# Kernel optimization log

Hardware: AMD Instinct MI355X
Metric: run time of the kernel (lower is better)

The kernel has to match this reference:

```python
import jax, jax.numpy as jnp
import numpy as np

N_NODES = 50000
N_EDGES = 1600000
DIM = 128          # input_dim == hidden_dim == embed_dim
N_LAYERS = 5
NEG_SLOPE = 0.2    # PyG GATv2Conv default


def setup_inputs() -> dict:
    key = jax.random.key(0)
    ks = jax.random.split(key, 8)
    s = 1.0 / np.sqrt(DIM)
    x = jax.random.normal(ks[0], (N_NODES, DIM), dtype=jnp.float32)
    edge_index = jax.random.randint(ks[1], (2, N_EDGES), 0, N_NODES, dtype=jnp.int64)
    # stacked per-layer params (all dims are 128 so layers stack cleanly)
    Wl = jax.random.normal(ks[2], (N_LAYERS, DIM, DIM), dtype=jnp.float32) * s
    bl = jax.random.normal(ks[3], (N_LAYERS, DIM), dtype=jnp.float32) * 0.01
    Wr = jax.random.normal(ks[4], (N_LAYERS, DIM, DIM), dtype=jnp.float32) * s
    br = jax.random.normal(ks[5], (N_LAYERS, DIM), dtype=jnp.float32) * 0.01
    att = jax.random.normal(ks[6], (N_LAYERS, DIM), dtype=jnp.float32) * s
    bias = jax.random.normal(ks[7], (N_LAYERS, DIM), dtype=jnp.float32) * 0.01
    return {"x": x, "edge_index": edge_index, "Wl": Wl, "bl": bl,
            "Wr": Wr, "br": br, "att": att, "bias": bias}


def _gatv2_layer(x, src, dst, Wl, bl, Wr, br, att, bias):
    # x: [N, D]; src/dst: [E'] (self loops already appended)
    n = x.shape[0]
    xl = x @ Wl + bl                      # [N, D]  (source transform; also the message)
    xr = x @ Wr + br                      # [N, D]  (target transform)
    # per-edge GATv2 score: att . LeakyReLU(xl[src] + xr[dst])
    e = jax.nn.leaky_relu(xl[src] + xr[dst], NEG_SLOPE) @ att   # [E']
    # numerically stable segment-softmax over incoming edges of each dst node
    m = jax.ops.segment_max(e, dst, num_segments=n)
    m = jnp.where(jnp.isfinite(m), m, jnp.zeros_like(m))
    p = jnp.exp(e - m[dst])
    z = jax.ops.segment_sum(p, dst, num_segments=n)
    alpha = p / jnp.maximum(z[dst], jnp.asarray(1e-16, p.dtype))  # [E']
    out = jax.ops.segment_sum(alpha[:, None] * xl[src], dst, num_segments=n)
    return out + bias


def reference(x, edge_index, Wl, bl, Wr, br, att, bias):
    n = x.shape[0]
    # PyG GATv2Conv default add_self_loops=True; edges identical across layers -> append once
    loop = jnp.arange(n, dtype=edge_index.dtype)
    src = jnp.concatenate([edge_index[0], loop])
    dst = jnp.concatenate([edge_index[1], loop])
    h = x
    for i in range(N_LAYERS):
        h = _gatv2_layer(h, src, dst, Wl[i], bl[i], Wr[i], br[i], att[i], bias[i])
        if i < N_LAYERS - 1:
            h = jax.nn.relu(h)
    # global_mean_pool with batch=None -> mean over all nodes, shape [1, embed_dim]
    return jnp.mean(h, axis=0, keepdims=True)
```

## Files before the change

### kernel.cpp

```cpp
#include <hip/hip_runtime.h>
#include <hip/hip_bf16.h>

#define N_NODES 50000
#define N_EDGES 1600000
#define DIM 128
#define N_LAYERS 5
#define NEG 0.2f

#define NBKT 196
#define BCAP_A 9472
#define PBLK 98
#define EPB 16384
#define SEGCAP 12288
#define SENT N_NODES
#define LOG2E 1.4426950408889634f

typedef unsigned short u16;
typedef unsigned char u8;
typedef unsigned int u32;
using short8 = __attribute__((ext_vector_type(8))) short;
using f32x4  = __attribute__((ext_vector_type(4))) float;
typedef float f32x2 __attribute__((ext_vector_type(2)));

union FragU { uint4 u; short8 s; };

__device__ __forceinline__ f32x2 bf2v(u32 u) {
    union { u32 i; float f; } lo, hi;
    lo.i = u << 16;
    hi.i = u & 0xffff0000u;
    f32x2 r; r.x = lo.f; r.y = hi.f;
    return r;
}
__device__ __forceinline__ u16 f2bf(float f) {
    union { float f; u32 u; } v; v.f = f;
    u32 r = v.u + 0x7fffu + ((v.u >> 16) & 1u);
    return (u16)(r >> 16);
}
__device__ __forceinline__ u32 pk2(float a, float b) {
    return (u32)f2bf(a) | ((u32)f2bf(b) << 16);
}
__device__ __forceinline__ int clampi(int v) {
    v = (v < 0) ? 0 : v;
    return (v >= N_NODES) ? (N_NODES - 1) : v;
}
template<int CTRL>
__device__ __forceinline__ float rradd(float v) {
    int t = __builtin_amdgcn_update_dpp(0, __float_as_int(v), CTRL, 0xF, 0xF, true);
    return v + __int_as_float(t);
}

__global__ void k_probe(const int* __restrict__ ei32, int* __restrict__ flags,
                        int* __restrict__ bcnt) {
    __shared__ int cnt;
    int t = threadIdx.x;
    if (t == 0) cnt = 0;
    __syncthreads();
    if (ei32[2 * t + 1] == 0) atomicAdd(&cnt, 1);
    if (t < NBKT) bcnt[t] = 0;
    __syncthreads();
    if (t == 0) flags[0] = (cnt >= 255) ? 1 : 0;
}

__device__ __forceinline__ int ldidx(const void* ei, long long i, int m64) {
    int v = m64 ? (int)(((const long long*)ei)[i]) : ((const int*)ei)[i];
    return clampi(v);
}

__global__ void k_cvt_x(const float* __restrict__ x, u16* __restrict__ xb) {
    int i = blockIdx.x * 256 + threadIdx.x;
    float2 v = *(const float2*)(x + (size_t)i * 2);
    ((u32*)xb)[i] = pk2(v.x, v.y);
}

__global__ void k_cvt_w(const float* __restrict__ Wl, const float* __restrict__ Wr,
                        uint4* __restrict__ Wtg) {
    int id = blockIdx.x * 256 + threadIdx.x;
    if (id >= N_LAYERS * 16 * 256) return;
    int l = id >> 12;
    int rem = id & 4095;
    int kc = rem >> 8;
    int n = rem & 255;
    const float* W = (n < 128) ? (Wl + (size_t)l * DIM * DIM + n)
                               : (Wr + (size_t)l * DIM * DIM + (n - 128));
    u16 c[8];
#pragma unroll
    for (int j = 0; j < 8; ++j) c[j] = f2bf(W[(size_t)(kc * 8 + j) * DIM]);
    uint4 o;
    o.x = (u32)c[0] | ((u32)c[1] << 16);
    o.y = (u32)c[2] | ((u32)c[3] << 16);
    o.z = (u32)c[4] | ((u32)c[5] << 16);
    o.w = (u32)c[6] | ((u32)c[7] << 16);
    Wtg[(size_t)l * 4096 + n * 16 + (kc ^ (n & 15))] = o;
}

__global__ __launch_bounds__(1024) void k_part(
    const void* __restrict__ ei, const int* __restrict__ flags,
    int* __restrict__ bcnt, u32* __restrict__ bpk)
{
    __shared__ u32 ebuf[EPB];
    __shared__ u8  bkb[EPB];
    __shared__ int lh[NBKT];
    __shared__ int lb[NBKT + 1];
    __shared__ int gst[NBKT];
    __shared__ int sc[256];

    const int tid = threadIdx.x;
    const int m64 = flags[0];
    const long long e0 = (long long)blockIdx.x * EPB;

    for (int i = tid; i < NBKT; i += 1024) lh[i] = 0;
    __syncthreads();

    u32 pay[16];
    u32 meta[16];
    int nv = 0;
#pragma unroll
    for (int i = 0; i < 16; ++i) {
        long long e = e0 + i * 1024 + tid;
        if (e < N_EDGES) {
            int s = ldidx(ei, e, m64);
            int d = ldidx(ei, (long long)N_EDGES + e, m64);
            int b = d >> 8;
            int rank = atomicAdd(&lh[b], 1);
            pay[i] = (u32)s | ((u32)(d & 255) << 16);
            meta[i] = (u32)b | ((u32)rank << 8);
            nv = i + 1;
        }
    }
    __syncthreads();

    if (tid < 256) sc[tid] = (tid < NBKT) ? lh[tid] : 0;
    __syncthreads();
    for (int off = 1; off < 256; off <<= 1) {
        int v = 0;
        if (tid < 256 && tid >= off) v = sc[tid - off];
        __syncthreads();
        if (tid < 256) sc[tid] += v;
        __syncthreads();
    }
    if (tid < NBKT) lb[tid] = sc[tid] - lh[tid];
    if (tid == 0) lb[NBKT] = 0;
    if (tid < NBKT) gst[tid] = atomicAdd(&bcnt[tid], lh[tid]);
    __syncthreads();

#pragma unroll
    for (int i = 0; i < 16; ++i) {
        if (i < nv) {
            int b = (int)(meta[i] & 255);
            int rank = (int)(meta[i] >> 8);
            int p = lb[b] + rank;
            ebuf[p] = pay[i];
            bkb[p] = (u8)b;
        }
    }
    __syncthreads();

    int total = (e0 + EPB <= N_EDGES) ? EPB : (int)(N_EDGES - e0);
    for (int i = tid; i < total; i += 1024) {
        int b = (int)bkb[i];
        int off = gst[b] + (i - lb[b]);
        if (off < BCAP_A)
            bpk[(size_t)b * BCAP_A + off] = ebuf[i];
    }
}

__global__ __launch_bounds__(256) void k_deg(
    const u32* __restrict__ bpk, const int* __restrict__ bcnt,
    const void* __restrict__ ei, const int* __restrict__ flags,
    int* __restrict__ row_off, int* __restrict__ btot)
{
    __shared__ int dh[256];
    __shared__ int sc[256];
    int b = blockIdx.x;
    int tid = threadIdx.x;
    dh[tid] = 0;
    __syncthreads();
    int cnt = bcnt[b];
    if (cnt <= BCAP_A) {
        for (int i = tid; i < cnt; i += 256)
            atomicAdd(&dh[(bpk[(size_t)b * BCAP_A + i] >> 16) & 255], 1);
    } else {
        int m64 = flags[0];
        for (long long e = tid; e < N_EDGES; e += 256) {
            int d = ldidx(ei, (long long)N_EDGES + e, m64);
            if ((d >> 8) == b) atomicAdd(&dh[d & 255], 1);
        }
    }
    __syncthreads();
    int d = b * 256 + tid;
    int v = 0;
    if (d < N_NODES) {
        v = (dh[tid] + 1 + 3) & ~3;
        if (v < 16) v = 16;
    }
    sc[tid] = v;
    __syncthreads();
    for (int off = 1; off < 256; off <<= 1) {
        int t = (tid >= off) ? sc[tid - off] : 0;
        __syncthreads();
        sc[tid] += t;
        __syncthreads();
    }
    if (d < N_NODES) row_off[d] = sc[tid] - v;
    if (tid == 255) btot[b] = sc[255];
}

__global__ void k_bscan(const int* __restrict__ btot, int* __restrict__ boff,
                        int* __restrict__ row_off) {
    __shared__ int sc[256];
    int tid = threadIdx.x;
    int v = (tid < NBKT) ? btot[tid] : 0;
    sc[tid] = v;
    __syncthreads();
    for (int off = 1; off < 256; off <<= 1) {
        int t = (tid >= off) ? sc[tid - off] : 0;
        __syncthreads();
        sc[tid] += t;
        __syncthreads();
    }
    if (tid < NBKT) boff[tid] = sc[tid] - v;
    if (tid == NBKT - 1) row_off[N_NODES] = sc[tid];
}

__global__ __launch_bounds__(256) void k_scat(
    const u32* __restrict__ bpk, const int* __restrict__ bcnt,
    int* __restrict__ row_off, const int* __restrict__ boff,
    const int* __restrict__ btot, u32* __restrict__ col,
    const void* __restrict__ ei, const int* __restrict__ flags)
{
    __shared__ u32 stage[SEGCAP];
    __shared__ int cur[256];
    int b = blockIdx.x;
    int tid = threadIdx.x;
    int d_lo = b * 256;
    int d_hi = d_lo + 256; if (d_hi > N_NODES) d_hi = N_NODES;
    int base0 = boff[b];
    int seglen = btot[b];
    if (seglen > SEGCAP) seglen = SEGCAP;

    int d = d_lo + tid;
    int rloc = 0;
    int ext = 0;
    if (d < d_hi) {
        rloc = row_off[d];
        ext = (d + 1 < d_hi) ? row_off[d + 1] : btot[b];
        if (ext > SEGCAP) ext = SEGCAP;
        if (rloc < SEGCAP) stage[rloc] = (u32)d * 256u;
        cur[tid] = rloc + 1;
    }
    __syncthreads();

    int cnt = bcnt[b];
    if (cnt <= BCAP_A) {
        for (int i = tid; i < cnt; i += 256) {
            u32 p = bpk[(size_t)b * BCAP_A + i];
            int pos = atomicAdd(&cur[(p >> 16) & 255], 1);
            if (pos < SEGCAP) stage[pos] = (p & 0xffffu) * 256u;
        }
    } else {
        int m64 = flags[0];
        for (long long e = tid; e < N_EDGES; e += 256) {
            int dd = ldidx(ei, (long long)N_EDGES + e, m64);
            if ((dd >> 8) == b) {
                int s = ldidx(ei, e, m64);
                int pos = atomicAdd(&cur[dd & 255], 1);
                if (pos < SEGCAP) stage[pos] = (u32)s * 256u;
            }
        }
    }
    __syncthreads();
    if (d < d_hi) {
        for (int i = cur[tid]; i < ext; ++i) stage[i] = (u32)SENT * 256u;
    }
    __syncthreads();
    for (int i = tid; i < seglen; i += 256)
        col[base0 + i] = stage[i];
    if (d < d_hi) row_off[d] = base0 + rloc;
}

__global__ __launch_bounds__(256) void k_mm(
    const u16* __restrict__ hb,
    const uint4* __restrict__ Wtg,
    const float* __restrict__ bl, const float* __restrict__ br,
    const float* __restrict__ att,
    u16* __restrict__ xlb,
    u16* __restrict__ xrb)
{
    __shared__ uint4 wsh[4096];
    const int tid = threadIdx.x;
#pragma unroll
    for (int i = 0; i < 16; ++i) wsh[tid + i * 256] = Wtg[tid + i * 256];

    const int wave = tid >> 6, lane = tid & 63;
    const int q = lane >> 4, nn = lane & 15;
    const int mA = blockIdx.x * 64 + wave * 16 + nn;

    FragU afr[4];
    const uint4 az = make_uint4(0, 0, 0, 0);
#pragma unroll
    for (int s = 0; s < 4; ++s)
        afr[s].u = (mA < N_NODES)
                 ? *(const uint4*)(hb + (size_t)mA * DIM + s * 32 + q * 8)
                 : az;
    __syncthreads();

    f32x4 acc[16];
#pragma unroll
    for (int i = 0; i < 16; ++i) acc[i] = (f32x4){0.f, 0.f, 0.f, 0.f};

#pragma unroll
    for (int s = 0; s < 4; ++s) {
#pragma unroll
        for (int nt = 0; nt < 16; ++nt) {
            int n = nt * 16 + nn;
            int kc = s * 4 + q;
            FragU b;
            b.u = wsh[n * 16 + (kc ^ (n & 15))];
            acc[nt] = __builtin_amdgcn_mfma_f32_16x16x32_bf16(afr[s].s, b.s, acc[nt], 0, 0, 0);
        }
    }

    const int mBase = blockIdx.x * 64 + wave * 16 + q * 4;
#pragma unroll
    for (int nt = 0; nt < 16; ++nt) {
        int n = nt * 16 + nn;
        bool isL = (n < 128);
        float bv = isL ? bl[n] : br[n - 128];
#pragma unroll
        for (int r = 0; r < 4; ++r) {
            int m = mBase + r;
            if (m < N_NODES) {
                float v = acc[nt][r] + bv;
                if (isL) xlb[(size_t)m * DIM + n] = f2bf(v);
                else     xrb[(size_t)m * DIM + (n - 128)] = f2bf(v);
            }
        }
    }

    if (blockIdx.x == 0 && tid < DIM) {
        float s = att[tid];
        xlb[(size_t)SENT * DIM + tid] = f2bf(s >= 0.f ? -10000.f : 10000.f);
    }
}

#define PROC(U) do {                                                          \
    f32x2 x01 = bf2v((U).x), x23 = bf2v((U).y);                               \
    f32x2 x45 = bf2v((U).z), x67 = bf2v((U).w);                               \
    f32x2 z01 = x01 + xr01, z23 = x23 + xr23;                                 \
    f32x2 z45 = x45 + xr45, z67 = x67 + xr67;                                 \
    f32x2 m01 = z01 * negv, m23 = z23 * negv;                                 \
    f32x2 m45 = z45 * negv, m67 = z67 * negv;                                 \
    z01.x = fmaxf(z01.x, m01.x); z01.y = fmaxf(z01.y, m01.y);                 \
    z23.x = fmaxf(z23.x, m23.x); z23.y = fmaxf(z23.y, m23.y);                 \
    z45.x = fmaxf(z45.x, m45.x); z45.y = fmaxf(z45.y, m45.y);                 \
    z67.x = fmaxf(z67.x, m67.x); z67.y = fmaxf(z67.y, m67.y);                 \
    f32x2 pp2 = at01 * z01;                                                   \
    pp2 = at23 * z23 + pp2;                                                   \
    pp2 = at45 * z45 + pp2;                                                   \
    pp2 = at67 * z67 + pp2;                                                   \
    float pp = pp2.x + pp2.y;                                                 \
    pp = rradd<0x121>(pp);                                                    \
    pp = rradd<0x122>(pp);                                                    \
    pp = rradd<0x124>(pp);                                                    \
    pp = rradd<0x128>(pp);                                                    \
    float w_ = exp2f(pp);                                                     \
    lsum += w_;                                                               \
    f32x2 wv; wv.x = w_; wv.y = w_;                                           \
    ac01 = wv * x01 + ac01; ac23 = wv * x23 + ac23;                           \
    ac45 = wv * x45 + ac45; ac67 = wv * x67 + ac67;                           \
} while (0)

#define LDQ(U, Q) do {                                                        \
    u32 ob_ = __shfl(off, ((Q) << 2) + g, 64);                                \
    (U) = *(const uint4*)(xbp + (size_t)(ob_ + dofs));                        \
} while (0)

template <int RELU>
__global__ __launch_bounds__(256) void k_edge(
    const u16* __restrict__ xlb, const u16* __restrict__ xrb,
    const int* __restrict__ row_off, const u32* __restrict__ col,
    const float* __restrict__ att, const float* __restrict__ bias,
    u16* __restrict__ hout)
{
    int gtid = blockIdx.x * 256 + threadIdx.x;
    int node = gtid >> 6;
    int lane = threadIdx.x & 63;
    int g = lane >> 4;
    int t = lane & 15;
    if (node >= N_NODES) return;

    const int d0 = t * 8;
    const u32 dofs = (u32)(t << 4);
    const char* xbp = (const char*)xlb;

    uint4 xru = *(const uint4*)(xrb + (size_t)node * DIM + d0);
    f32x2 xr01 = bf2v(xru.x), xr23 = bf2v(xru.y), xr45 = bf2v(xru.z), xr67 = bf2v(xru.w);
    float2 a0 = *(const float2*)(att + d0);
    float2 a1 = *(const float2*)(att + d0 + 2);
    float2 a2 = *(const float2*)(att + d0 + 4);
    float2 a3 = *(const float2*)(att + d0 + 6);
    f32x2 at01, at23, at45, at67;
    at01.x = a0.x * LOG2E; at01.y = a0.y * LOG2E;
    at23.x = a1.x * LOG2E; at23.y = a1.y * LOG2E;
    at45.x = a2.x * LOG2E; at45.y = a2.y * LOG2E;
    at67.x = a3.x * LOG2E; at67.y = a3.y * LOG2E;
    f32x2 negv; negv.x = NEG; negv.y = NEG;

    const int beg = __builtin_amdgcn_readfirstlane(row_off[node]);
    const int end = __builtin_amdgcn_readfirstlane(row_off[node + 1]);
    const int n = end - beg;
    const int nreg = (n < 64) ? n : 64;
    const int nq = nreg >> 2;

    u32 off = col[beg + lane];

    f32x2 ac01, ac23, ac45, ac67;
    ac01.x = ac01.y = ac23.x = ac23.y = 0.f;
    ac45.x = ac45.y = ac67.x = ac67.y = 0.f;
    float lsum = 0.f;

    uint4 u0, u1, u2, u3;
    LDQ(u0, 0); LDQ(u1, 1); LDQ(u2, 2); LDQ(u3, 3);

    int q = 0;
    for (; q + 8 <= nq; q += 4) {
        PROC(u0); LDQ(u0, q + 4);
        PROC(u1); LDQ(u1, q + 5);
        PROC(u2); LDQ(u2, q + 6);
        PROC(u3); LDQ(u3, q + 7);
    }
    PROC(u0); if (q + 4 < nq) LDQ(u0, q + 4);
    PROC(u1); if (q + 5 < nq) LDQ(u1, q + 5);
    PROC(u2); if (q + 6 < nq) LDQ(u2, q + 6);
    PROC(u3); if (q + 7 < nq) LDQ(u3, q + 7);
    q += 4;
    if (q     < nq) PROC(u0);
    if (q + 1 < nq) PROC(u1);
    if (q + 2 < nq) PROC(u2);

    for (int j = beg + 64 + g; j < end; j += 4) {
        u32 ob_ = col[j];
        uint4 u = *(const uint4*)(xbp + (size_t)(ob_ + dofs));
        PROC(u);
    }

    float accv[8] = {ac01.x, ac01.y, ac23.x, ac23.y, ac45.x, ac45.y, ac67.x, ac67.y};
#pragma unroll
    for (int i = 0; i < 8; ++i) {
        accv[i] += __shfl_xor(accv[i], 16, 64);
        accv[i] += __shfl_xor(accv[i], 32, 64);
    }
    lsum += __shfl_xor(lsum, 16, 64);
    lsum += __shfl_xor(lsum, 32, 64);

    if (g == 0) {
        float inv = 1.f / fmaxf(lsum, 1e-16f);
        float4 b0 = *(const float4*)(bias + d0);
        float4 b1 = *(const float4*)(bias + d0 + 4);
        float o0 = accv[0] * inv + b0.x;
        float o1 = accv[1] * inv + b0.y;
        float o2 = accv[2] * inv + b0.z;
        float o3 = accv[3] * inv + b0.w;
        float o4 = accv[4] * inv + b1.x;
        float o5 = accv[5] * inv + b1.y;
        float o6 = accv[6] * inv + b1.z;
        float o7 = accv[7] * inv + b1.w;
        if (RELU) {
            o0 = fmaxf(o0, 0.f); o1 = fmaxf(o1, 0.f);
            o2 = fmaxf(o2, 0.f); o3 = fmaxf(o3, 0.f);
            o4 = fmaxf(o4, 0.f); o5 = fmaxf(o5, 0.f);
            o6 = fmaxf(o6, 0.f); o7 = fmaxf(o7, 0.f);
        }
        uint4 o;
        o.x = pk2(o0, o1);
        o.y = pk2(o2, o3);
        o.z = pk2(o4, o5);
        o.w = pk2(o6, o7);
        *(uint4*)(hout + (size_t)node * DIM + d0) = o;
    }
}

__global__ void k_mean_part(const u16* __restrict__ hb, float* __restrict__ part) {
    int d = threadIdx.x;
    int b = blockIdx.x;
    int n0 = b * 200;
    float s = 0.f;
    for (int i = 0; i < 200; ++i) {
        union { u32 i; float f; } v;
        v.i = (u32)hb[(size_t)(n0 + i) * DIM + d] << 16;
        s += v.f;
    }
    part[b * DIM + d] = s;
}

__global__ void k_mean_final(const float* __restrict__ part, float* __restrict__ out) {
    int d = threadIdx.x;
    float s = 0.f;
    for (int b = 0; b < 250; ++b) s += part[b * DIM + d];
    out[d] = s * (1.f / (float)N_NODES);
}

extern "C" void kernel_launch(void* const* d_in, const int* in_sizes, int n_in,
                              void* d_out, int out_size, void* d_ws, size_t ws_size,
                              hipStream_t stream) {
    int ix, iei, iWl, ibl, iWr, ibr, iatt, ibias;
    if (in_sizes[0] == N_NODES * DIM) {
        ix = 0; iei = 1; iWl = 2; ibl = 3; iWr = 4; ibr = 5; iatt = 6; ibias = 7;
    } else {
        iWl = 0; iWr = 1; iatt = 2; ibias = 3; ibl = 4; ibr = 5; iei = 6; ix = 7;
    }
    const float* x    = (const float*)d_in[ix];
    const void*  ei   = d_in[iei];
    const float* Wl   = (const float*)d_in[iWl];
    const float* bl   = (const float*)d_in[ibl];
    const float* Wr   = (const float*)d_in[iWr];
    const float* br   = (const float*)d_in[ibr];
    const float* att  = (const float*)d_in[iatt];
    const float* bias = (const float*)d_in[ibias];
    float* out = (float*)d_out;

    char* w = (char*)d_ws;
    float* part = (float*)w;      w += (size_t)256 * DIM * 4;
    uint4* Wtg = (uint4*)w;       w += (size_t)N_LAYERS * 4096 * 16;
    u16* xb  = (u16*)w;           w += (size_t)N_NODES * DIM * 2;
    u16* hb  = (u16*)w;           w += (size_t)N_NODES * DIM * 2;
    u16* xlb = (u16*)w;           w += (size_t)(N_NODES + 1) * DIM * 2;
    u16* xrb = (u16*)w;           w += (size_t)N_NODES * DIM * 2;
    int* row_off = (int*)w;       w += (size_t)(N_NODES + 4) * 4;
    int* flags = (int*)w;         w += 64;
    int* bcnt = (int*)w;          w += (size_t)(NBKT + 4) * 4;
    int* btot = (int*)w;          w += (size_t)(NBKT + 4) * 4;
    int* boff = (int*)w;          w += (size_t)(NBKT + 4) * 4;
    u32* bpk = (u32*)w;           w += (size_t)NBKT * BCAP_A * 4;
    u32* col = (u32*)w;           w += (size_t)(N_EDGES + 8 * N_NODES + 64) * 4;

    k_probe<<<1, 256, 0, stream>>>((const int*)ei, flags, bcnt);
    k_cvt_x<<<(N_NODES * DIM / 2 + 255) / 256, 256, 0, stream>>>(x, xb);
    k_cvt_w<<<(N_LAYERS * 4096 + 255) / 256, 256, 0, stream>>>(Wl, Wr, Wtg);
    k_part<<<PBLK, 1024, 0, stream>>>(ei, flags, bcnt, bpk);
    k_deg<<<NBKT, 256, 0, stream>>>(bpk, bcnt, ei, flags, row_off, btot);
    k_bscan<<<1, 256, 0, stream>>>(btot, boff, row_off);
    k_scat<<<NBKT, 256, 0, stream>>>(bpk, bcnt, row_off, boff, btot, col, ei, flags);

    const int mm_grid = (N_NODES + 63) / 64;
    const int edge_grid = (N_NODES * 64 + 255) / 256;

    for (int layer = 0; layer < N_LAYERS; ++layer) {
        const uint4* Wp = Wtg + (size_t)layer * 4096;
        const float* blp = bl + (size_t)layer * DIM;
        const float* brp = br + (size_t)layer * DIM;
        const float* ap  = att + (size_t)layer * DIM;
        const float* bp  = bias + (size_t)layer * DIM;

        const u16* hin = (layer == 0) ? xb : hb;
        k_mm<<<mm_grid, 256, 0, stream>>>(hin, Wp, blp, brp, ap, xlb, xrb);

        if (layer < N_LAYERS - 1)
            k_edge<1><<<edge_grid, 256, 0, stream>>>(xlb, xrb, row_off, col, ap, bp, hb);
        else
            k_edge<0><<<edge_grid, 256, 0, stream>>>(xlb, xrb, row_off, col, ap, bp, hb);
    }

    k_mean_part<<<250, 128, 0, stream>>>(hb, part);
    k_mean_final<<<1, 128, 0, stream>>>(part, out);
}
```

Before: 573.0 us.

## Process four nodes per wavefront in edge kernel with prefetched row offsets

Each wavefront now handles four consecutive destination nodes instead of one, and the grid shrinks to match. While one node is processed, the row offsets and first column indices of the next node are prefetched, hiding that index-load latency. This cuts the number of waves launched and the repeated setup such as loading att. The cost is less parallelism per node and a longer serial chain per wave, which may lower latency hiding for the gathers.

Measured after the change: 590.4 us. 1.03x slower.

```diff
diff --git a/kernel.cpp b/kernel.cpp
--- a/kernel.cpp
+++ b/kernel.cpp
@@ -382,19 +382,14 @@
     const float* __restrict__ att, const float* __restrict__ bias,
     u16* __restrict__ hout)
 {
-    int gtid = blockIdx.x * 256 + threadIdx.x;
-    int node = gtid >> 6;
-    int lane = threadIdx.x & 63;
-    int g = lane >> 4;
-    int t = lane & 15;
-    if (node >= N_NODES) return;
-
+    const int wid = blockIdx.x * 4 + (threadIdx.x >> 6);
+    const int lane = threadIdx.x & 63;
+    const int g = lane >> 4;
+    const int t = lane & 15;
     const int d0 = t * 8;
     const u32 dofs = (u32)(t << 4);
     const char* xbp = (const char*)xlb;
 
-    uint4 xru = *(const uint4*)(xrb + (size_t)node * DIM + d0);
-    f32x2 xr01 = bf2v(xru.x), xr23 = bf2v(xru.y), xr45 = bf2v(xru.z), xr67 = bf2v(xru.w);
     float2 a0 = *(const float2*)(att + d0);
     float2 a1 = *(const float2*)(att + d0 + 2);
     float2 a2 = *(const float2*)(att + d0 + 4);
@@ -406,77 +401,95 @@
     at67.x = a3.x * LOG2E; at67.y = a3.y * LOG2E;
     f32x2 negv; negv.x = NEG; negv.y = NEG;
 
-    const int beg = __builtin_amdgcn_readfirstlane(row_off[node]);
-    const int end = __builtin_amdgcn_readfirstlane(row_off[node + 1]);
-    const int n = end - beg;
-    const int nreg = (n < 64) ? n : 64;
-    const int nq = nreg >> 2;
-
+    int nid = wid * 4;
+    int beg = __builtin_amdgcn_readfirstlane(row_off[nid]);
+    int end = __builtin_amdgcn_readfirstlane(row_off[nid + 1]);
     u32 off = col[beg + lane];
 
-    f32x2 ac01, ac23, ac45, ac67;
-    ac01.x = ac01.y = ac23.x = ac23.y = 0.f;
-    ac45.x = ac45.y = ac67.x = ac67.y = 0.f;
-    float lsum = 0.f;
-
-    uint4 u0, u1, u2, u3;
-    LDQ(u0, 0); LDQ(u1, 1); LDQ(u2, 2); LDQ(u3, 3);
-
-    int q = 0;
-    for (; q + 8 <= nq; q += 4) {
-        PROC(u0); LDQ(u0, q + 4);
-        PROC(u1); LDQ(u1, q + 5);
-        PROC(u2); LDQ(u2, q + 6);
-        PROC(u3); LDQ(u3, q + 7);
-    }
-    PROC(u0); if (q + 4 < nq) LDQ(u0, q + 4);
-    PROC(u1); if (q + 5 < nq) LDQ(u1, q + 5);
-    PROC(u2); if (q + 6 < nq) LDQ(u2, q + 6);
-    PROC(u3); if (q + 7 < nq) LDQ(u3, q + 7);
-    q += 4;
-    if (q     < nq) PROC(u0);
-    if (q + 1 < nq) PROC(u1);
-    if (q + 2 < nq) PROC(u2);
-
-    for (int j = beg + 64 + g; j < end; j += 4) {
-        u32 ob_ = col[j];
-        uint4 u = *(const uint4*)(xbp + (size_t)(ob_ + dofs));
-        PROC(u);
-    }
-
-    float accv[8] = {ac01.x, ac01.y, ac23.x, ac23.y, ac45.x, ac45.y, ac67.x, ac67.y};
-#pragma unroll
-    for (int i = 0; i < 8; ++i) {
-        accv[i] += __shfl_xor(accv[i], 16, 64);
-        accv[i] += __shfl_xor(accv[i], 32, 64);
-    }
-    lsum += __shfl_xor(lsum, 16, 64);
-    lsum += __shfl_xor(lsum, 32, 64);
-
-    if (g == 0) {
-        float inv = 1.f / fmaxf(lsum, 1e-16f);
-        float4 b0 = *(const float4*)(bias + d0);
-        float4 b1 = *(const float4*)(bias + d0 + 4);
-        float o0 = accv[0] * inv + b0.x;
-        float o1 = accv[1] * inv + b0.y;
-        float o2 = accv[2] * inv + b0.z;
-        float o3 = accv[3] * inv + b0.w;
-        float o4 = accv[4] * inv + b1.x;
-        float o5 = accv[5] * inv + b1.y;
-        float o6 = accv[6] * inv + b1.z;
-        float o7 = accv[7] * inv + b1.w;
-        if (RELU) {
-            o0 = fmaxf(o0, 0.f); o1 = fmaxf(o1, 0.f);
-            o2 = fmaxf(o2, 0.f); o3 = fmaxf(o3, 0.f);
-            o4 = fmaxf(o4, 0.f); o5 = fmaxf(o5, 0.f);
-            o6 = fmaxf(o6, 0.f); o7 = fmaxf(o7, 0.f);
-        }
-        uint4 o;
-        o.x = pk2(o0, o1);
-        o.y = pk2(o2, o3);
-        o.z = pk2(o4, o5);
-        o.w = pk2(o6, o7);
-        *(uint4*)(hout + (size_t)node * DIM + d0) = o;
+    for (int i = 0; i < 4; ++i) {
+        const int nidN = nid + 1;
+        int begN = 0, endN = 0;
+        if (i < 3) {
+            begN = __builtin_amdgcn_readfirstlane(row_off[nidN]);
+            endN = __builtin_amdgcn_readfirstlane(row_off[nidN + 1]);
+        }
+        uint4 xru = *(const uint4*)(xrb + (size_t)nid * DIM + d0);
+        u32 offN = 0;
+        if (i < 3) offN = col[begN + lane];
+
+        f32x2 xr01 = bf2v(xru.x), xr23 = bf2v(xru.y);
+        f32x2 xr45 = bf2v(xru.z), xr67 = bf2v(xru.w);
+
+        const int n = end - beg;
+        const int nreg = (n < 64) ? n : 64;
+        const int nq = nreg >> 2;
+
+        f32x2 ac01, ac23, ac45, ac67;
+        ac01.x = ac01.y = ac23.x = ac23.y = 0.f;
+        ac45.x = ac45.y = ac67.x = ac67.y = 0.f;
+        float lsum = 0.f;
+
+        uint4 u0, u1, u2, u3;
+        LDQ(u0, 0); LDQ(u1, 1); LDQ(u2, 2); LDQ(u3, 3);
+
+        int q = 0;
+        for (; q + 8 <= nq; q += 4) {
+            PROC(u0); LDQ(u0, q + 4);
+            PROC(u1); LDQ(u1, q + 5);
+            PROC(u2); LDQ(u2, q + 6);
+            PROC(u3); LDQ(u3, q + 7);
+        }
+        PROC(u0); if (q + 4 < nq) LDQ(u0, q + 4);
+        PROC(u1); if (q + 5 < nq) LDQ(u1, q + 5);
+        PROC(u2); if (q + 6 < nq) LDQ(u2, q + 6);
+        PROC(u3); if (q + 7 < nq) LDQ(u3, q + 7);
+        q += 4;
+        if (q     < nq) PROC(u0);
+        if (q + 1 < nq) PROC(u1);
+        if (q + 2 < nq) PROC(u2);
+
+        for (int j = beg + 64 + g; j < end; j += 4) {
+            u32 ob_ = col[j];
+            uint4 u = *(const uint4*)(xbp + (size_t)(ob_ + dofs));
+            PROC(u);
+        }
+
+        float accv[8] = {ac01.x, ac01.y, ac23.x, ac23.y, ac45.x, ac45.y, ac67.x, ac67.y};
+#pragma unroll
+        for (int k = 0; k < 8; ++k) {
+            accv[k] += __shfl_xor(accv[k], 16, 64);
+            accv[k] += __shfl_xor(accv[k], 32, 64);
+        }
+        lsum += __shfl_xor(lsum, 16, 64);
+        lsum += __shfl_xor(lsum, 32, 64);
+
+        if (g == 0) {
+            float inv = 1.f / fmaxf(lsum, 1e-16f);
+            float4 b0 = *(const float4*)(bias + d0);
+            float4 b1 = *(const float4*)(bias + d0 + 4);
+            float o0 = accv[0] * inv + b0.x;
+            float o1 = accv[1] * inv + b0.y;
+            float o2 = accv[2] * inv + b0.z;
+            float o3 = accv[3] * inv + b0.w;
+            float o4 = accv[4] * inv + b1.x;
+            float o5 = accv[5] * inv + b1.y;
+            float o6 = accv[6] * inv + b1.z;
+            float o7 = accv[7] * inv + b1.w;
+            if (RELU) {
+                o0 = fmaxf(o0, 0.f); o1 = fmaxf(o1, 0.f);
+                o2 = fmaxf(o2, 0.f); o3 = fmaxf(o3, 0.f);
+                o4 = fmaxf(o4, 0.f); o5 = fmaxf(o5, 0.f);
+                o6 = fmaxf(o6, 0.f); o7 = fmaxf(o7, 0.f);
+            }
+            uint4 o;
+            o.x = pk2(o0, o1);
+            o.y = pk2(o2, o3);
+            o.z = pk2(o4, o5);
+            o.w = pk2(o6, o7);
+            *(uint4*)(hout + (size_t)nid * DIM + d0) = o;
+        }
+
+        nid = nidN; beg = begN; end = endN; off = offN;
     }
 }
 
@@ -543,7 +556,7 @@
     k_scat<<<NBKT, 256, 0, stream>>>(bpk, bcnt, row_off, boff, btot, col, ei, flags);
 
     const int mm_grid = (N_NODES + 63) / 64;
-    const int edge_grid = (N_NODES * 64 + 255) / 256;
+    const int edge_grid = 3125;
 
     for (int layer = 0; layer < N_LAYERS; ++layer) {
         const uint4* Wp = Wtg + (size_t)layer * 4096;
```
